# Optimization experiments

Measured on AMD Instinct MI355X. Metric: run time of the kernel, lower is better.

## Reference

```python
import jax, jax.numpy as jnp
import numpy as np

D_MODEL = 1024
N_HEAD = 16
D_FF = 4096
SEQ = 2048
BATCH = 4
EPS = 1e-5


def setup_inputs() -> dict:
    key = jax.random.key(0)
    ks = jax.random.split(key, 10)
    s = 0.02
    return {
        "src": jax.random.normal(ks[0], (SEQ, BATCH, D_MODEL), jnp.float32),
        "padding_mask": jnp.zeros((BATCH, SEQ), jnp.bool_),
        "w_qkv": jax.random.normal(ks[1], (3 * D_MODEL, D_MODEL), jnp.float32) * s,
        "fc_w": jax.random.normal(ks[2], (D_MODEL, D_MODEL), jnp.float32) * s,
        "fc_b": jnp.zeros((D_MODEL,), jnp.float32),
        "w1": jax.random.normal(ks[3], (D_FF, D_MODEL), jnp.float32) * s,
        "b1": jnp.zeros((D_FF,), jnp.float32),
        "w2": jax.random.normal(ks[4], (D_MODEL, D_FF), jnp.float32) * s,
        "b2": jnp.zeros((D_MODEL,), jnp.float32),
        "g1": jnp.ones((D_MODEL,), jnp.float32),
        "be1": jnp.zeros((D_MODEL,), jnp.float32),
        "g2": jnp.ones((D_MODEL,), jnp.float32),
        "be2": jnp.zeros((D_MODEL,), jnp.float32),
    }


def _layer_norm(x, g, b):
    mu = jnp.mean(x, axis=-1, keepdims=True)
    var = jnp.mean(jnp.square(x - mu), axis=-1, keepdims=True)
    return (x - mu) * jax.lax.rsqrt(var + EPS) * g + b


def _mha(src, padding_mask, w_qkv, fc_w, fc_b):
    L, B, D = src.shape
    H = N_HEAD
    dh = D // H
    qkv = jnp.einsum("lbd,ed->lbe", src, w_qkv)  # (L,B,3D)
    q, k, v = jnp.split(qkv, 3, axis=-1)
    # (L, B*H, dh) -> (B*H, L, dh)
    q = q.reshape(L, B * H, dh).transpose(1, 0, 2)
    k = k.reshape(L, B * H, dh).transpose(1, 0, 2)
    v = v.reshape(L, B * H, dh).transpose(1, 0, 2)
    scores = jnp.einsum("nqd,nkd->nqk", q, k) / np.sqrt(dh).astype(np.float32)
    scores = scores.reshape(B, H, L, L)
    scores = jnp.where(padding_mask[:, None, None, :], -jnp.inf, scores)
    attn = jax.nn.softmax(scores, axis=-1).reshape(B * H, L, L)
    out = jnp.einsum("nqk,nkd->nqd", attn, v)  # (B*H, L, dh)
    out = out.transpose(1, 0, 2).reshape(L, B, D)
    return out @ fc_w.T + fc_b


def reference(src, padding_mask, w_qkv, fc_w, fc_b, w1, b1, w2, b2, g1, be1, g2, be2):
    src2 = _mha(src, padding_mask, w_qkv, fc_w, fc_b)
    src = _layer_norm(src + src2, g1, be1)
    h = jax.nn.relu(src @ w1.T + b1)
    src2 = h @ w2.T + b2
    return _layer_norm(src + src2, g2, be2)
```

## Files before the change

### kernel.cpp

```cpp
#include <hip/hip_runtime.h>
#include <cstdint>
#include <cstddef>

typedef __attribute__((ext_vector_type(8))) short bf16x8;
typedef __attribute__((ext_vector_type(4))) float f32x4;
typedef __attribute__((ext_vector_type(16))) float f32x16;

static __device__ __forceinline__ unsigned short f2bf(float f) {
    union { float f; unsigned u; } v; v.f = f;
    unsigned r = v.u + 0x7FFFu + ((v.u >> 16) & 1u);
    return (unsigned short)(r >> 16);
}
static __device__ __forceinline__ float bf2f(unsigned short u) {
    union { unsigned u; float f; } v; v.u = ((unsigned)u) << 16; return v.f;
}

static __device__ __forceinline__ void gld_lds16(const void* g, void* l) {
    unsigned loff = (unsigned)(size_t)l;
    loff = (unsigned)__builtin_amdgcn_readfirstlane((int)loff);
    __builtin_amdgcn_global_load_lds(
        (const __attribute__((address_space(1))) unsigned int*)(size_t)g,
        (__attribute__((address_space(3))) unsigned int*)(size_t)loff,
        16, 0, 0);
}

__global__ __launch_bounds__(256) void k_cvt5(
    const float* __restrict__ p0, const float* __restrict__ p1,
    const float* __restrict__ p2, const float* __restrict__ p3,
    const float* __restrict__ p4,
    unsigned short* __restrict__ q0, unsigned short* __restrict__ q1,
    unsigned short* __restrict__ q2, unsigned short* __restrict__ q3,
    unsigned short* __restrict__ q4)
{
    const int blk = blockIdx.x;
    const float* in; unsigned short* out; int base;
    if      (blk < 3072)  { in = p0; out = q0; base = blk; }
    else if (blk < 4096)  { in = p1; out = q1; base = blk - 3072; }
    else if (blk < 8192)  { in = p2; out = q2; base = blk - 4096; }
    else if (blk < 12288) { in = p3; out = q3; base = blk - 8192; }
    else                  { in = p4; out = q4; base = blk - 12288; }
    const int i = (base * 256 + threadIdx.x) * 4;
    float4 v = *reinterpret_cast<const float4*>(in + i);
    ushort4 o;
    o.x = f2bf(v.x); o.y = f2bf(v.y); o.z = f2bf(v.z); o.w = f2bf(v.w);
    *reinterpret_cast<ushort4*>(out + i) = o;
}

template<int BM, int MF>
__global__ __launch_bounds__(512, 2) void k_gemm8(
    const unsigned short* __restrict__ A, const unsigned short* __restrict__ W,
    float* __restrict__ Cf, unsigned short* __restrict__ Cb,
    const float* __restrict__ bias,
    int M, int N, int K, int scale_cols, float scale, int relu)
{
    __shared__ unsigned short As[2][BM * 64];
    __shared__ unsigned short Bs[2][256 * 64];
    const int tid = threadIdx.x, wid = tid >> 6, lane = tid & 63;
    const int lr = lane & 15, g16 = (lane >> 4) * 16;
    const int wm = wid >> 2, wn = wid & 3;

    const int nbx = N >> 8;
    const int nwg = gridDim.x;
    const int raw = blockIdx.x;
    const int swz = (raw & 7) * (nwg >> 3) + (raw >> 3);
    const int bm = (swz / nbx) * BM, bn = (swz % nbx) * 256;

    const int rin = tid >> 3;
    const int cole = (((tid & 7) * 16) ^ ((rin & 7) << 4)) >> 1;

    auto STAGE = [&](int bb, int kt1) {
        #pragma unroll
        for (int c = 0; c < BM / 64; ++c)
            gld_lds16(A + (size_t)(bm + c * 64 + rin) * K + kt1 + cole,
                      (char*)As[bb] + c * 8192 + wid * 1024);
        #pragma unroll
        for (int c = 0; c < 4; ++c)
            gld_lds16(W + (size_t)(bn + c * 64 + rin) * K + kt1 + cole,
                      (char*)Bs[bb] + c * 8192 + wid * 1024);
    };

    f32x4 acc[MF][4] = {};

    STAGE(0, 0);
    STAGE(1, 64);
    int cur = 0;

    for (int kt = 0; kt < K; kt += 64) {
        if (kt + 64 < K) {
            if constexpr (BM == 256) asm volatile("s_waitcnt vmcnt(8)" ::: "memory");
            else                     asm volatile("s_waitcnt vmcnt(6)" ::: "memory");
        } else {
            asm volatile("s_waitcnt vmcnt(0)" ::: "memory");
        }
        __builtin_amdgcn_s_barrier();

        const char* Ab = (const char*)As[cur];
        const char* Bb = (const char*)Bs[cur];
        bf16x8 bfr[4][2];

        #pragma unroll
        for (int p = 0; p < MF / 2; ++p) {
            bf16x8 af[2][2];
            #pragma unroll
            for (int mi = 0; mi < 2; ++mi)
                #pragma unroll
                for (int kk = 0; kk < 2; ++kk) {
                    const int row = wm * (MF * 16) + (2 * p + mi) * 16 + lr;
                    af[mi][kk] = *reinterpret_cast<const bf16x8*>(
                        Ab + row * 128 + ((kk * 64 + g16) ^ ((row & 7) << 4)));
                }
            if (p == 0) {
                #pragma unroll
                for (int n = 0; n < 4; ++n)
                    #pragma unroll
                    for (int kk = 0; kk < 2; ++kk) {
                        const int row = wn * 64 + n * 16 + lr;
                        bfr[n][kk] = *reinterpret_cast<const bf16x8*>(
                            Bb + row * 128 + ((kk * 64 + g16) ^ ((row & 7) << 4)));
                    }
            }
            __builtin_amdgcn_s_barrier();
            __builtin_amdgcn_s_setprio(1);
            #pragma unroll
            for (int mi = 0; mi < 2; ++mi)
                #pragma unroll
                for (int n = 0; n < 4; ++n)
                    #pragma unroll
                    for (int kk = 0; kk < 2; ++kk)
                        acc[2 * p + mi][n] = __builtin_amdgcn_mfma_f32_16x16x32_bf16(
                            af[mi][kk], bfr[n][kk], acc[2 * p + mi][n], 0, 0, 0);
            __builtin_amdgcn_s_setprio(0);
            __builtin_amdgcn_s_barrier();
        }
        if (kt + 128 < K) STAGE(cur, kt + 128);
        cur ^= 1;
    }

    #pragma unroll
    for (int m = 0; m < MF; ++m) {
        #pragma unroll
        for (int n = 0; n < 4; ++n) {
            const int col = bn + wn * 64 + n * 16 + lr;
            const float bv = bias ? bias[col] : 0.0f;
            const float sc = (col < scale_cols) ? scale : 1.0f;
            #pragma unroll
            for (int r = 0; r < 4; ++r) {
                const int row = bm + wm * (MF * 16) + m * 16 + (lane >> 4) * 4 + r;
                float v = acc[m][n][r] * sc + bv;
                if (relu) v = fmaxf(v, 0.0f);
                if (Cb) Cb[(size_t)row * N + col] = f2bf(v);
                else    Cf[(size_t)row * N + col] = v;
            }
        }
    }
}

__global__ __launch_bounds__(256) void k_vtrans(
    const unsigned short* __restrict__ qkv, unsigned short* __restrict__ vt)
{
    __shared__ unsigned short T[64][72];
    const int n = blockIdx.y, b = n >> 4, h = n & 15;
    const int l0 = blockIdx.x * 64;
    const int tid = threadIdx.x;
    {
        const int l = tid >> 2, d = (tid & 3) * 16;
        const unsigned short* p = qkv + (size_t)(l0 + l) * 12288 + b * 3072 + 2048 + h * 64 + d;
        *reinterpret_cast<bf16x8*>(&T[l][d])     = *reinterpret_cast<const bf16x8*>(p);
        *reinterpret_cast<bf16x8*>(&T[l][d + 8]) = *reinterpret_cast<const bf16x8*>(p + 8);
    }
    __syncthreads();
    {
        const int d = tid >> 2, lc = (tid & 3) * 16;
        unsigned short tmp[16];
        #pragma unroll
        for (int j = 0; j < 16; ++j) tmp[j] = T[lc + j][d];
        unsigned short* q = vt + ((size_t)n * 64 + d) * 2048 + l0 + lc;
        *reinterpret_cast<bf16x8*>(q)     = *reinterpret_cast<bf16x8*>(tmp);
        *reinterpret_cast<bf16x8*>(q + 8) = *reinterpret_cast<bf16x8*>(tmp + 8);
    }
}

__global__ __launch_bounds__(256) void k_attn(
    const unsigned short* __restrict__ qkv,
    const unsigned short* __restrict__ vt,
    const unsigned char* __restrict__ mask,
    unsigned short* __restrict__ out)
{
    __shared__ unsigned short Ks[2][64 * 64];
    __shared__ unsigned short Vs[2][64 * 64];
    const int tid = threadIdx.x, wid = tid >> 6, lane = tid & 63;
    const int q32 = lane & 31, hi = lane >> 5;
    const int raw = blockIdx.x;
    const int swz = (raw & 7) * 128 + (raw >> 3);
    const int n = swz >> 4, qblk = swz & 15;
    const int b = n >> 4, h = n & 15;
    const int qbase = qblk * 128 + wid * 32;
    const size_t SL = 12288;

    bf16x8 qf[4];
    {
        const unsigned short* qrow = qkv + (size_t)(qbase + q32) * SL + (size_t)b * 3072 + h * 64;
        #pragma unroll
        for (int t = 0; t < 4; ++t)
            qf[t] = *reinterpret_cast<const bf16x8*>(qrow + t * 16 + hi * 8);
    }

    bool anym;
    {
        const uint4* mp = reinterpret_cast<const uint4*>(mask + b * 2048);
        uint4 m0 = mp[lane * 2], m1 = mp[lane * 2 + 1];
        unsigned mo = m0.x | m0.y | m0.z | m0.w | m1.x | m1.y | m1.z | m1.w;
        anym = __any(mo != 0);
    }

    const int sw = (q32 & 7) << 4;
    int koff[4], voff[2][2];
    #pragma unroll
    for (int t = 0; t < 4; ++t) koff[t] = q32 * 128 + ((t * 32 + hi * 16) ^ sw);
    #pragma unroll
    for (int ks = 0; ks < 2; ++ks)
        #pragma unroll
        for (int hf = 0; hf < 2; ++hf)
            voff[ks][hf] = q32 * 128 + ((ks * 64 + hf * 32 + hi * 16) ^ sw);

    const int soff = wid * 1024 + lane * 16;
    const int srow0 = soff >> 7;
    const int sbc0  = (soff & 127) ^ ((srow0 & 7) << 4);
    const int srow1 = (soff + 4096) >> 7;
    const int sbc1  = ((soff + 4096) & 127) ^ ((srow1 & 7) << 4);
    const unsigned short* kgbase = qkv + (size_t)b * 3072 + 1024 + h * 64;
    const unsigned short* vgbase = vt + (size_t)n * 64 * 2048;

    #define STAGE(buf, kt)                                                            \
        do {                                                                          \
            gld_lds16(kgbase + (size_t)((kt) + srow0) * SL + (sbc0 >> 1),             \
                      (char*)Ks[buf] + wid * 1024);                                   \
            gld_lds16(vgbase + (size_t)srow0 * 2048 + (kt) + (sbc0 >> 1),             \
                      (char*)Vs[buf] + wid * 1024);                                   \
            gld_lds16(kgbase + (size_t)((kt) + srow1) * SL + (sbc1 >> 1),             \
                      (char*)Ks[buf] + 4096 + wid * 1024);                            \
            gld_lds16(vgbase + (size_t)srow1 * 2048 + (kt) + (sbc1 >> 1),             \
                      (char*)Vs[buf] + 4096 + wid * 1024);                            \
        } while (0)

    f32x16 o0 = {}, o1 = {}, o2 = {};
    union { unsigned w[4]; bf16x8 v; } onesf;
    onesf.w[0] = 0x3F803F80u; onesf.w[1] = 0x3F803F80u;
    onesf.w[2] = 0x3F803F80u; onesf.w[3] = 0x3F803F80u;

    STAGE(0, 0);
    int cur = 0;

    for (int kt = 0; kt < 2048; kt += 64) {
        __syncthreads();
        if (kt + 64 < 2048) STAGE(cur ^ 1, kt + 64);
        const char* Kb = (const char*)Ks[cur];
        const char* Vb = (const char*)Vs[cur];

        #pragma unroll
        for (int ks = 0; ks < 2; ++ks) {
            f32x16 s = {};
            __builtin_amdgcn_s_setprio(1);
            #pragma unroll
            for (int t = 0; t < 4; ++t) {
                const bf16x8 kf = *reinterpret_cast<const bf16x8*>(Kb + ks * 4096 + koff[t]);
                s = __builtin_amdgcn_mfma_f32_32x32x16_bf16(kf, qf[t], s, 0, 0, 0);
            }
            __builtin_amdgcn_s_setprio(0);

            if (anym) {
                #pragma unroll
                for (int r = 0; r < 16; ++r) {
                    const int kl = (r & 3) + 8 * (r >> 2) + 4 * hi;
                    if (mask[b * 2048 + kt + ks * 32 + kl]) s[r] = -3e8f;
                }
            }

            #pragma unroll
            for (int i = 0; i < 16; ++i) s[i] = exp2f(s[i] - 8.0f);

            unsigned pk[8];
            #pragma unroll
            for (int i = 0; i < 8; ++i)
                asm("v_cvt_pk_bf16_f32 %0, %1, %2" : "=v"(pk[i]) : "v"(s[2 * i]), "v"(s[2 * i + 1]));
            asm("v_permlane32_swap_b32 %0, %1" : "+v"(pk[2]), "+v"(pk[0]));
            asm("v_permlane32_swap_b32 %0, %1" : "+v"(pk[3]), "+v"(pk[1]));
            asm("v_permlane32_swap_b32 %0, %1" : "+v"(pk[6]), "+v"(pk[4]));
            asm("v_permlane32_swap_b32 %0, %1" : "+v"(pk[7]), "+v"(pk[5]));
            union { unsigned w[4]; bf16x8 v; } pb0, pb1;
            pb0.w[0] = pk[0]; pb0.w[1] = pk[1]; pb0.w[2] = pk[2]; pb0.w[3] = pk[3];
            pb1.w[0] = pk[4]; pb1.w[1] = pk[5]; pb1.w[2] = pk[6]; pb1.w[3] = pk[7];

            const bf16x8 v00 = *reinterpret_cast<const bf16x8*>(Vb + voff[ks][0]);
            const bf16x8 v01 = *reinterpret_cast<const bf16x8*>(Vb + voff[ks][1]);
            const bf16x8 v10 = *reinterpret_cast<const bf16x8*>(Vb + 4096 + voff[ks][0]);
            const bf16x8 v11 = *reinterpret_cast<const bf16x8*>(Vb + 4096 + voff[ks][1]);
            __builtin_amdgcn_s_setprio(1);
            o0 = __builtin_amdgcn_mfma_f32_32x32x16_bf16(v00, pb0.v, o0, 0, 0, 0);
            o0 = __builtin_amdgcn_mfma_f32_32x32x16_bf16(v01, pb1.v, o0, 0, 0, 0);
            o1 = __builtin_amdgcn_mfma_f32_32x32x16_bf16(v10, pb0.v, o1, 0, 0, 0);
            o1 = __builtin_amdgcn_mfma_f32_32x32x16_bf16(v11, pb1.v, o1, 0, 0, 0);
            o2 = __builtin_amdgcn_mfma_f32_32x32x16_bf16(onesf.v, pb0.v, o2, 0, 0, 0);
            o2 = __builtin_amdgcn_mfma_f32_32x32x16_bf16(onesf.v, pb1.v, o2, 0, 0, 0);
            __builtin_amdgcn_s_setprio(0);
        }
        cur ^= 1;
    }
    #undef STAGE

    const float rl = 1.0f / o2[0];
    unsigned short* orow = out + ((size_t)(qbase + q32) * 4 + b) * 1024 + h * 64;
    #pragma unroll
    for (int q4 = 0; q4 < 4; ++q4) {
        unsigned w0, w1, w2, w3;
        asm("v_cvt_pk_bf16_f32 %0, %1, %2" : "=v"(w0) : "v"(o0[q4 * 4 + 0] * rl), "v"(o0[q4 * 4 + 1] * rl));
        asm("v_cvt_pk_bf16_f32 %0, %1, %2" : "=v"(w1) : "v"(o0[q4 * 4 + 2] * rl), "v"(o0[q4 * 4 + 3] * rl));
        asm("v_cvt_pk_bf16_f32 %0, %1, %2" : "=v"(w2) : "v"(o1[q4 * 4 + 0] * rl), "v"(o1[q4 * 4 + 1] * rl));
        asm("v_cvt_pk_bf16_f32 %0, %1, %2" : "=v"(w3) : "v"(o1[q4 * 4 + 2] * rl), "v"(o1[q4 * 4 + 3] * rl));
        uint2 ua; ua.x = w0; ua.y = w1;
        uint2 ub; ub.x = w2; ub.y = w3;
        *reinterpret_cast<uint2*>(orow + q4 * 8 + hi * 4)      = ua;
        *reinterpret_cast<uint2*>(orow + 32 + q4 * 8 + hi * 4) = ub;
    }
}

__global__ __launch_bounds__(256) void k_add_ln_fb(
    const float* __restrict__ x, const unsigned short* __restrict__ y,
    const float* __restrict__ gamma, const float* __restrict__ beta,
    unsigned short* __restrict__ outb)
{
    const int row = blockIdx.x * 4 + (threadIdx.x >> 6);
    const int lane = threadIdx.x & 63;
    const size_t base = (size_t)row * 1024;
    float v[16];
    float s = 0.0f, ss = 0.0f;
    #pragma unroll
    for (int i = 0; i < 4; ++i) {
        const int c = lane * 4 + i * 256;
        float4 a = *reinterpret_cast<const float4*>(x + base + c);
        ushort4 d = *reinterpret_cast<const ushort4*>(y + base + c);
        v[i * 4 + 0] = a.x + bf2f(d.x); v[i * 4 + 1] = a.y + bf2f(d.y);
        v[i * 4 + 2] = a.z + bf2f(d.z); v[i * 4 + 3] = a.w + bf2f(d.w);
        #pragma unroll
        for (int j = 0; j < 4; ++j) { s += v[i * 4 + j]; ss += v[i * 4 + j] * v[i * 4 + j]; }
    }
    #pragma unroll
    for (int o = 1; o < 64; o <<= 1) { s += __shfl_xor(s, o); ss += __shfl_xor(ss, o); }
    const float mu = s * (1.0f / 1024.0f);
    const float var = ss * (1.0f / 1024.0f) - mu * mu;
    const float rstd = rsqrtf(var + 1e-5f);
    #pragma unroll
    for (int i = 0; i < 4; ++i) {
        const int c = lane * 4 + i * 256;
        float4 gq = *reinterpret_cast<const float4*>(gamma + c);
        float4 bq = *reinterpret_cast<const float4*>(beta + c);
        ushort4 ob;
        ob.x = f2bf((v[i * 4 + 0] - mu) * rstd * gq.x + bq.x);
        ob.y = f2bf((v[i * 4 + 1] - mu) * rstd * gq.y + bq.y);
        ob.z = f2bf((v[i * 4 + 2] - mu) * rstd * gq.z + bq.z);
        ob.w = f2bf((v[i * 4 + 3] - mu) * rstd * gq.w + bq.w);
        *reinterpret_cast<ushort4*>(outb + base + c) = ob;
    }
}

__global__ __launch_bounds__(256) void k_add_ln_bb(
    const unsigned short* __restrict__ x, const unsigned short* __restrict__ y,
    const float* __restrict__ gamma, const float* __restrict__ beta,
    float* __restrict__ outf)
{
    const int row = blockIdx.x * 4 + (threadIdx.x >> 6);
    const int lane = threadIdx.x & 63;
    const size_t base = (size_t)row * 1024;
    float v[16];
    float s = 0.0f, ss = 0.0f;
    #pragma unroll
    for (int i = 0; i < 4; ++i) {
        const int c = lane * 4 + i * 256;
        ushort4 a = *reinterpret_cast<const ushort4*>(x + base + c);
        ushort4 d = *reinterpret_cast<const ushort4*>(y + base + c);
        v[i * 4 + 0] = bf2f(a.x) + bf2f(d.x); v[i * 4 + 1] = bf2f(a.y) + bf2f(d.y);
        v[i * 4 + 2] = bf2f(a.z) + bf2f(d.z); v[i * 4 + 3] = bf2f(a.w) + bf2f(d.w);
        #pragma unroll
        for (int j = 0; j < 4; ++j) { s += v[i * 4 + j]; ss += v[i * 4 + j] * v[i * 4 + j]; }
    }
    #pragma unroll
    for (int o = 1; o < 64; o <<= 1) { s += __shfl_xor(s, o); ss += __shfl_xor(ss, o); }
    const float mu = s * (1.0f / 1024.0f);
    const float var = ss * (1.0f / 1024.0f) - mu * mu;
    const float rstd = rsqrtf(var + 1e-5f);
    #pragma unroll
    for (int i = 0; i < 4; ++i) {
        const int c = lane * 4 + i * 256;
        float4 gq = *reinterpret_cast<const float4*>(gamma + c);
        float4 bq = *reinterpret_cast<const float4*>(beta + c);
        float4 o;
        o.x = (v[i * 4 + 0] - mu) * rstd * gq.x + bq.x;
        o.y = (v[i * 4 + 1] - mu) * rstd * gq.y + bq.y;
        o.z = (v[i * 4 + 2] - mu) * rstd * gq.z + bq.z;
        o.w = (v[i * 4 + 3] - mu) * rstd * gq.w + bq.w;
        *reinterpret_cast<float4*>(outf + base + c) = o;
    }
}

extern "C" void kernel_launch(void* const* d_in, const int* in_sizes, int n_in,
                              void* d_out, int out_size, void* d_ws, size_t ws_size,
                              hipStream_t stream) {
    const float* src  = (const float*)d_in[0];
    const unsigned char* mask = (const unsigned char*)d_in[1];
    const float* w_qkv = (const float*)d_in[2];
    const float* fc_w = (const float*)d_in[3];
    const float* fc_b = (const float*)d_in[4];
    const float* w1   = (const float*)d_in[5];
    const float* b1   = (const float*)d_in[6];
    const float* w2   = (const float*)d_in[7];
    const float* b2   = (const float*)d_in[8];
    const float* g1   = (const float*)d_in[9];
    const float* be1  = (const float*)d_in[10];
    const float* g2   = (const float*)d_in[11];
    const float* be2  = (const float*)d_in[12];
    float* out = (float*)d_out;

    char* ws = (char*)d_ws;
    size_t o = 0;
    auto take = [&](size_t nbytes) { size_t p = o; o += (nbytes + 255) & ~(size_t)255; return p; };
    unsigned short* wqkv_b = (unsigned short*)(ws + take((size_t)3072 * 1024 * 2));
    unsigned short* fcw_b  = (unsigned short*)(ws + take((size_t)1024 * 1024 * 2));
    unsigned short* w1_b   = (unsigned short*)(ws + take((size_t)4096 * 1024 * 2));
    unsigned short* w2_b   = (unsigned short*)(ws + take((size_t)1024 * 4096 * 2));
    unsigned short* src_b  = (unsigned short*)(ws + take((size_t)8192 * 1024 * 2));
    unsigned short* qkv_b  = (unsigned short*)(ws + take((size_t)8192 * 3072 * 2));
    unsigned short* attn_b = (unsigned short*)(ws + take((size_t)8192 * 1024 * 2));
    unsigned short* h_b    = (unsigned short*)(ws + take((size_t)8192 * 4096 * 2));
    unsigned short* proj_b = qkv_b;
    unsigned short* y_b    = qkv_b;
    unsigned short* x1_b   = src_b;
    unsigned short* vt_b   = h_b;

    k_cvt5<<<dim3(20480), 256, 0, stream>>>(w_qkv, fc_w, w1, w2, src,
                                            wqkv_b, fcw_b, w1_b, w2_b, src_b);

    k_gemm8<256, 8><<<dim3((8192 / 256) * (3072 / 256)), 512, 0, stream>>>(
        src_b, wqkv_b, nullptr, qkv_b, nullptr, 8192, 3072, 1024, 1024, 0.18033688011112042f, 0);

    k_vtrans<<<dim3(32, 64), 256, 0, stream>>>(qkv_b, vt_b);

    k_attn<<<dim3(1024), 256, 0, stream>>>(qkv_b, vt_b, mask, attn_b);

    k_gemm8<128, 4><<<dim3((8192 / 128) * (1024 / 256)), 512, 0, stream>>>(
        attn_b, fcw_b, nullptr, proj_b, fc_b, 8192, 1024, 1024, 0, 1.0f, 0);

    k_add_ln_fb<<<dim3(8192 / 4), 256, 0, stream>>>(src, proj_b, g1, be1, x1_b);

    k_gemm8<256, 8><<<dim3((8192 / 256) * (4096 / 256)), 512, 0, stream>>>(
        x1_b, w1_b, nullptr, h_b, b1, 8192, 4096, 1024, 0, 1.0f, 1);

    k_gemm8<128, 4><<<dim3((8192 / 128) * (1024 / 256)), 512, 0, stream>>>(
        h_b, w2_b, nullptr, y_b, b2, 8192, 1024, 4096, 0, 1.0f, 0);

    k_add_ln_bb<<<dim3(8192 / 4), 256, 0, stream>>>(x1_b, y_b, g2, be2, out);
}
```

Baseline: 437.1 us.

## Widen attention blocks to 8 waves sharing K/V tiles; use bf16 residual in LN1

The attention kernel now runs 512-thread blocks covering 256 queries, so each staged 64-key K/V tile is shared by twice as many waves. Each thread issues half as many async global-to-LDS loads. The softmax exponent drops the constant -8 shift and calls the raw hardware exp2 builtin, which cuts ALU work but leaves less headroom against overflow. The first add+LayerNorm reads the bf16 copy of src instead of fp32, halving its residual read traffic at a small precision cost. The two LayerNorm kernels are merged into one template.

```diff
diff --git a/kernel.cpp b/kernel.cpp
--- a/kernel.cpp
+++ b/kernel.cpp
@@ -180,7 +180,7 @@
     }
 }
 
-__global__ __launch_bounds__(256) void k_attn(
+__global__ __launch_bounds__(512) void k_attn(
     const unsigned short* __restrict__ qkv,
     const unsigned short* __restrict__ vt,
     const unsigned char* __restrict__ mask,
@@ -191,10 +191,10 @@
     const int tid = threadIdx.x, wid = tid >> 6, lane = tid & 63;
     const int q32 = lane & 31, hi = lane >> 5;
     const int raw = blockIdx.x;
-    const int swz = (raw & 7) * 128 + (raw >> 3);
-    const int n = swz >> 4, qblk = swz & 15;
+    const int swz = (raw & 7) * 64 + (raw >> 3);
+    const int n = swz >> 3, qblk = swz & 7;
     const int b = n >> 4, h = n & 15;
-    const int qbase = qblk * 128 + wid * 32;
+    const int qbase = qblk * 256 + wid * 32;
     const size_t SL = 12288;
 
     bf16x8 qf[4];
@@ -224,23 +224,17 @@
             voff[ks][hf] = q32 * 128 + ((ks * 64 + hf * 32 + hi * 16) ^ sw);
 
     const int soff = wid * 1024 + lane * 16;
-    const int srow0 = soff >> 7;
-    const int sbc0  = (soff & 127) ^ ((srow0 & 7) << 4);
-    const int srow1 = (soff + 4096) >> 7;
-    const int sbc1  = ((soff + 4096) & 127) ^ ((srow1 & 7) << 4);
+    const int srow = soff >> 7;
+    const int sbc  = (soff & 127) ^ ((srow & 7) << 4);
     const unsigned short* kgbase = qkv + (size_t)b * 3072 + 1024 + h * 64;
     const unsigned short* vgbase = vt + (size_t)n * 64 * 2048;
 
     #define STAGE(buf, kt)                                                            \
         do {                                                                          \
-            gld_lds16(kgbase + (size_t)((kt) + srow0) * SL + (sbc0 >> 1),             \
+            gld_lds16(kgbase + (size_t)((kt) + srow) * SL + (sbc >> 1),               \
                       (char*)Ks[buf] + wid * 1024);                                   \
-            gld_lds16(vgbase + (size_t)srow0 * 2048 + (kt) + (sbc0 >> 1),             \
+            gld_lds16(vgbase + (size_t)srow * 2048 + (kt) + (sbc >> 1),               \
                       (char*)Vs[buf] + wid * 1024);                                   \
-            gld_lds16(kgbase + (size_t)((kt) + srow1) * SL + (sbc1 >> 1),             \
-                      (char*)Ks[buf] + 4096 + wid * 1024);                            \
-            gld_lds16(vgbase + (size_t)srow1 * 2048 + (kt) + (sbc1 >> 1),             \
-                      (char*)Vs[buf] + 4096 + wid * 1024);                            \
         } while (0)
 
     f32x16 o0 = {}, o1 = {}, o2 = {};
@@ -277,7 +271,7 @@
             }
 
             #pragma unroll
-            for (int i = 0; i < 16; ++i) s[i] = exp2f(s[i] - 8.0f);
+            for (int i = 0; i < 16; ++i) s[i] = __builtin_amdgcn_exp2f(s[i]);
 
             unsigned pk[8];
             #pragma unroll
@@ -324,10 +318,11 @@
     }
 }
 
-__global__ __launch_bounds__(256) void k_add_ln_fb(
-    const float* __restrict__ x, const unsigned short* __restrict__ y,
+template<int OUTF>
+__global__ __launch_bounds__(256) void k_add_ln(
+    const unsigned short* __restrict__ x, const unsigned short* __restrict__ y,
     const float* __restrict__ gamma, const float* __restrict__ beta,
-    unsigned short* __restrict__ outb)
+    float* __restrict__ outf, unsigned short* __restrict__ outb)
 {
     const int row = blockIdx.x * 4 + (threadIdx.x >> 6);
     const int lane = threadIdx.x & 63;
@@ -337,10 +332,10 @@
     #pragma unroll
     for (int i = 0; i < 4; ++i) {
         const int c = lane * 4 + i * 256;
-        float4 a = *reinterpret_cast<const float4*>(x + base + c);
+        ushort4 a = *reinterpret_cast<const ushort4*>(x + base + c);
         ushort4 d = *reinterpret_cast<const ushort4*>(y + base + c);
-        v[i * 4 + 0] = a.x + bf2f(d.x); v[i * 4 + 1] = a.y + bf2f(d.y);
-        v[i * 4 + 2] = a.z + bf2f(d.z); v[i * 4 + 3] = a.w + bf2f(d.w);
+        v[i * 4 + 0] = bf2f(a.x) + bf2f(d.x); v[i * 4 + 1] = bf2f(a.y) + bf2f(d.y);
+        v[i * 4 + 2] = bf2f(a.z) + bf2f(d.z); v[i * 4 + 3] = bf2f(a.w) + bf2f(d.w);
         #pragma unroll
         for (int j = 0; j < 4; ++j) { s += v[i * 4 + j]; ss += v[i * 4 + j] * v[i * 4 + j]; }
     }
@@ -354,51 +349,18 @@
         const int c = lane * 4 + i * 256;
         float4 gq = *reinterpret_cast<const float4*>(gamma + c);
         float4 bq = *reinterpret_cast<const float4*>(beta + c);
-        ushort4 ob;
-        ob.x = f2bf((v[i * 4 + 0] - mu) * rstd * gq.x + bq.x);
-        ob.y = f2bf((v[i * 4 + 1] - mu) * rstd * gq.y + bq.y);
-        ob.z = f2bf((v[i * 4 + 2] - mu) * rstd * gq.z + bq.z);
-        ob.w = f2bf((v[i * 4 + 3] - mu) * rstd * gq.w + bq.w);
-        *reinterpret_cast<ushort4*>(outb + base + c) = ob;
-    }
-}
-
-__global__ __launch_bounds__(256) void k_add_ln_bb(
-    const unsigned short* __restrict__ x, const unsigned short* __restrict__ y,
-    const float* __restrict__ gamma, const float* __restrict__ beta,
-    float* __restrict__ outf)
-{
-    const int row = blockIdx.x * 4 + (threadIdx.x >> 6);
-    const int lane = threadIdx.x & 63;
-    const size_t base = (size_t)row * 1024;
-    float v[16];
-    float s = 0.0f, ss = 0.0f;
-    #pragma unroll
-    for (int i = 0; i < 4; ++i) {
-        const int c = lane * 4 + i * 256;
-        ushort4 a = *reinterpret_cast<const ushort4*>(x + base + c);
-        ushort4 d = *reinterpret_cast<const ushort4*>(y + base + c);
-        v[i * 4 + 0] = bf2f(a.x) + bf2f(d.x); v[i * 4 + 1] = bf2f(a.y) + bf2f(d.y);
-        v[i * 4 + 2] = bf2f(a.z) + bf2f(d.z); v[i * 4 + 3] = bf2f(a.w) + bf2f(d.w);
-        #pragma unroll
-        for (int j = 0; j < 4; ++j) { s += v[i * 4 + j]; ss += v[i * 4 + j] * v[i * 4 + j]; }
-    }
-    #pragma unroll
-    for (int o = 1; o < 64; o <<= 1) { s += __shfl_xor(s, o); ss += __shfl_xor(ss, o); }
-    const float mu = s * (1.0f / 1024.0f);
-    const float var = ss * (1.0f / 1024.0f) - mu * mu;
-    const float rstd = rsqrtf(var + 1e-5f);
-    #pragma unroll
-    for (int i = 0; i < 4; ++i) {
-        const int c = lane * 4 + i * 256;
-        float4 gq = *reinterpret_cast<const float4*>(gamma + c);
-        float4 bq = *reinterpret_cast<const float4*>(beta + c);
-        float4 o;
-        o.x = (v[i * 4 + 0] - mu) * rstd * gq.x + bq.x;
-        o.y = (v[i * 4 + 1] - mu) * rstd * gq.y + bq.y;
-        o.z = (v[i * 4 + 2] - mu) * rstd * gq.z + bq.z;
-        o.w = (v[i * 4 + 3] - mu) * rstd * gq.w + bq.w;
-        *reinterpret_cast<float4*>(outf + base + c) = o;
+        float o0 = (v[i * 4 + 0] - mu) * rstd * gq.x + bq.x;
+        float o1 = (v[i * 4 + 1] - mu) * rstd * gq.y + bq.y;
+        float o2 = (v[i * 4 + 2] - mu) * rstd * gq.z + bq.z;
+        float o3 = (v[i * 4 + 3] - mu) * rstd * gq.w + bq.w;
+        if (OUTF) {
+            float4 o; o.x = o0; o.y = o1; o.z = o2; o.w = o3;
+            *reinterpret_cast<float4*>(outf + base + c) = o;
+        } else {
+            ushort4 ob;
+            ob.x = f2bf(o0); ob.y = f2bf(o1); ob.z = f2bf(o2); ob.w = f2bf(o3);
+            *reinterpret_cast<ushort4*>(outb + base + c) = ob;
+        }
     }
 }
 
@@ -444,12 +406,12 @@
 
     k_vtrans<<<dim3(32, 64), 256, 0, stream>>>(qkv_b, vt_b);
 
-    k_attn<<<dim3(1024), 256, 0, stream>>>(qkv_b, vt_b, mask, attn_b);
+    k_attn<<<dim3(512), 512, 0, stream>>>(qkv_b, vt_b, mask, attn_b);
 
     k_gemm8<128, 4><<<dim3((8192 / 128) * (1024 / 256)), 512, 0, stream>>>(
         attn_b, fcw_b, nullptr, proj_b, fc_b, 8192, 1024, 1024, 0, 1.0f, 0);
 
-    k_add_ln_fb<<<dim3(8192 / 4), 256, 0, stream>>>(src, proj_b, g1, be1, x1_b);
+    k_add_ln<0><<<dim3(8192 / 4), 256, 0, stream>>>(src_b, proj_b, g1, be1, nullptr, x1_b);
 
     k_gemm8<256, 8><<<dim3((8192 / 256) * (4096 / 256)), 512, 0, stream>>>(
         x1_b, w1_b, nullptr, h_b, b1, 8192, 4096, 1024, 0, 1.0f, 1);
@@ -457,5 +419,5 @@
     k_gemm8<128, 4><<<dim3((8192 / 128) * (1024 / 256)), 512, 0, stream>>>(
         h_b, w2_b, nullptr, y_b, b2, 8192, 1024, 4096, 0, 1.0f, 0);
 
-    k_add_ln_bb<<<dim3(8192 / 4), 256, 0, stream>>>(x1_b, y_b, g2, be2, out);
-}
+    k_add_ln<1><<<dim3(8192 / 4), 256, 0, stream>>>(x1_b, y_b, g2, be2, out, nullptr);
+}
```

After: 408.3 us. -6.6%, faster.
